# Kernel tuning notes

Measured on AMD Instinct MI355X. Metric: run time of the kernel, lower is better.

Reference implementation:

```python
import jax, jax.numpy as jnp
import numpy as np


def setup_inputs() -> dict:
    key = jax.random.key(0)
    doc_embeddings = jax.random.normal(key, (16384, 128), dtype=jnp.float32)
    return {"doc_embeddings": doc_embeddings}


def reference(doc_embeddings) -> jnp.ndarray:
    n = doc_embeddings.shape[0]
    # [N, N] pairwise dot products
    scores = jnp.matmul(doc_embeddings, doc_embeddings.T)
    positive_scores = jnp.diagonal(scores)  # [N]
    # zero out the diagonal (matches dot - eye*dot in the torch code)
    diag_mask = jnp.eye(n, dtype=scores.dtype)
    negative_scores = scores - diag_mask * scores
    positive_loss = jax.nn.log_sigmoid(positive_scores)            # [N]
    negative_loss = jax.nn.log_sigmoid(-negative_scores).sum(axis=1)  # [N]
    loss = -(positive_loss + negative_loss).mean()
    return loss
```

## Files before the change

### kernel.cpp

```cpp
#include <hip/hip_runtime.h>
#include <hip/hip_bf16.h>


#define N_DOCS 16384
#define DIM 128
#define NTILE 128
#define NTRI (NTILE * (NTILE + 1) / 2)
#define PBLOCKS 768

typedef __attribute__((ext_vector_type(4))) float f32x4;
typedef __attribute__((ext_vector_type(8))) __bf16 bf16x8;
typedef __attribute__((ext_vector_type(2))) long longx2;

typedef const __attribute__((address_space(1))) unsigned char* gptr_t;
typedef __attribute__((address_space(3))) unsigned char* lptr_t;

#define SQRT_LOG2E 1.2011224087864498f
#define LN2F 0.6931471805599453f
#define QC0 1.33985f
#define QC1 (-0.33985f)

#if __has_builtin(__builtin_amdgcn_exp2f)
#define EXP2F(x) __builtin_amdgcn_exp2f(x)
#else
#define EXP2F(x) exp2f(x)
#endif

#if __has_builtin(__builtin_amdgcn_mfma_scale_f32_16x16x128_f8f6f4)
#define HAVE_MX 1
typedef __attribute__((ext_vector_type(8))) int i32x8;
#endif

#define BARRIER() do { asm volatile("" ::: "memory"); \
                       __builtin_amdgcn_s_barrier();  \
                       asm volatile("" ::: "memory"); } while (0)

__device__ __forceinline__ unsigned short f2bf(float f) {
  unsigned int u = __float_as_uint(f);
  u += 0x7fffu + ((u >> 16) & 1u);
  return (unsigned short)(u >> 16);
}

#if __has_builtin(__builtin_amdgcn_cvt_pk_fp8_f32)
#define HAVE_CVT_FP8 1
#else
__device__ __forceinline__ unsigned char f2e4m3(float x) {
  unsigned int u = __float_as_uint(x);
  unsigned char sgn = (unsigned char)((u >> 31) << 7);
  float ax = fabsf(x);
  if (!(ax < 464.f)) return sgn | 0x7E;
  unsigned int ua = u & 0x7FFFFFFFu;
  int e = (int)(ua >> 23) - 127;
  if (e < -6) {
    float q = rintf(ax * 512.f);
    return sgn | (unsigned char)q;
  }
  unsigned int mant = ua & 0x7FFFFFu;
  unsigned int keep = mant >> 20;
  unsigned int rest = mant & 0xFFFFFu;
  keep += (rest > 0x80000u) || (rest == 0x80000u && (keep & 1u));
  unsigned int ee = (unsigned int)(e + 7);
  if (keep == 8u) { keep = 0u; ee++; }
  if (ee >= 16u) return sgn | 0x7E;
  return sgn | (unsigned char)((ee << 3) | keep);
}
#endif

__device__ __forceinline__ void tri_decode(int g, int& tr, int& tc) {
  int r = (int)((2 * NTILE + 1 -
                 sqrtf((float)((2 * NTILE + 1) * (2 * NTILE + 1)) - 8.0f * (float)g)) * 0.5f);
  while (r * NTILE - r * (r - 1) / 2 > g) --r;
  while ((r + 1) * NTILE - (r + 1) * r / 2 <= g) ++r;
  tr = r;
  tc = r + (g - (r * NTILE - r * (r - 1) / 2));
}

__global__ __launch_bounds__(256) void cast_kernel(const float* __restrict__ in,
                                                   unsigned char* __restrict__ out,
                                                   float* __restrict__ rpart,
                                                   float* __restrict__ colpart,
                                                   float* __restrict__ accum,
                                                   unsigned int* __restrict__ counter) {
  __shared__ float cs[16][136];
  __shared__ float redr[4];
  const int b = blockIdx.x, tid = threadIdx.x;
  const int kb = tid & 15, rg = tid >> 4;
  if (b == 0 && tid == 0) { accum[0] = 0.f; *counter = 0u; }

  float csum[8] = {0.f, 0.f, 0.f, 0.f, 0.f, 0.f, 0.f, 0.f};
  float rsum = 0.f;
#pragma unroll
  for (int it = 0; it < 8; ++it) {
    int r = it * 16 + rg;
    int row = b * 128 + r;
    const float4* p = reinterpret_cast<const float4*>(in + (size_t)row * 128 + kb * 8);
    float4 a = p[0], c = p[1];
    float v0 = a.x * SQRT_LOG2E, v1 = a.y * SQRT_LOG2E, v2 = a.z * SQRT_LOG2E,
          v3 = a.w * SQRT_LOG2E, v4 = c.x * SQRT_LOG2E, v5 = c.y * SQRT_LOG2E,
          v6 = c.z * SQRT_LOG2E, v7 = c.w * SQRT_LOG2E;
    int w0, w1;
#ifdef HAVE_CVT_FP8
    w0 = __builtin_amdgcn_cvt_pk_fp8_f32(v0, v1, 0, false);
    w0 = __builtin_amdgcn_cvt_pk_fp8_f32(v2, v3, w0, true);
    w1 = __builtin_amdgcn_cvt_pk_fp8_f32(v4, v5, 0, false);
    w1 = __builtin_amdgcn_cvt_pk_fp8_f32(v6, v7, w1, true);
#else
    w0 = (int)f2e4m3(v0) | ((int)f2e4m3(v1) << 8) | ((int)f2e4m3(v2) << 16) | ((int)f2e4m3(v3) << 24);
    w1 = (int)f2e4m3(v4) | ((int)f2e4m3(v5) << 8) | ((int)f2e4m3(v6) << 16) | ((int)f2e4m3(v7) << 24);
#endif
    int g = kb & 3, s = kb >> 2;
    int off = b * 16384 + (g * 2 + (s >> 1)) * 2048 + r * 16 + (s & 1) * 8;
    *reinterpret_cast<int2*>(out + off) = make_int2(w0, w1);
    csum[0] += v0; csum[1] += v1; csum[2] += v2; csum[3] += v3;
    csum[4] += v4; csum[5] += v5; csum[6] += v6; csum[7] += v7;
    rsum = fmaf(v0, v0, rsum); rsum = fmaf(v1, v1, rsum);
    rsum = fmaf(v2, v2, rsum); rsum = fmaf(v3, v3, rsum);
    rsum = fmaf(v4, v4, rsum); rsum = fmaf(v5, v5, rsum);
    rsum = fmaf(v6, v6, rsum); rsum = fmaf(v7, v7, rsum);
  }
#pragma unroll
  for (int j = 0; j < 8; ++j) cs[rg][kb * 8 + j] = csum[j];
#pragma unroll
  for (int off = 32; off > 0; off >>= 1) rsum += __shfl_down(rsum, off);
  if ((tid & 63) == 0) redr[tid >> 6] = rsum;
  __syncthreads();
  if (tid < 128) {
    float s = 0.f;
#pragma unroll
    for (int r = 0; r < 16; ++r) s += cs[r][tid];
    colpart[b * 128 + tid] = s;
  }
  if (tid == 0) rpart[b] = redr[0] + redr[1] + redr[2] + redr[3];
}

__global__ __launch_bounds__(512, 6) void loss_persist(const unsigned char* __restrict__ ef8,
                                                       float* __restrict__ accum,
                                                       unsigned int* __restrict__ counter,
                                                       const float* __restrict__ rpart,
                                                       const float* __restrict__ colpart,
                                                       float* __restrict__ out) {
  __shared__ alignas(16) unsigned char Asl[16384];
  __shared__ alignas(16) unsigned char Bsl[2][16384];
  __shared__ float red[8];
  __shared__ int lastFlag;
  const int tid = threadIdx.x;
  const int p = blockIdx.x;
  const int g0 = (p * 43) >> 2;
  const int g1 = ((p + 1) * 43) >> 2;
  const int n = g1 - g0;

  const int wid = tid >> 6;
  const int lane = tid & 63;
  const int wm = wid >> 2, wn = wid & 3;
  const int lrow = lane & 15;
  const int kgrp = lane >> 4;

  auto stageA = [&](int t) {
    const unsigned char* s = ef8 + (size_t)t * 16384;
#pragma unroll
    for (int it = 0; it < 2; ++it) {
      int pp = (it * 512 + tid) * 16;
      __builtin_amdgcn_global_load_lds((gptr_t)(s + pp), (lptr_t)(Asl + pp), 16, 0, 0);
    }
  };
  auto stageB = [&](int t, int buf) {
    const unsigned char* s = ef8 + (size_t)t * 16384;
#pragma unroll
    for (int it = 0; it < 2; ++it) {
      int pp = (it * 512 + tid) * 16;
      __builtin_amdgcn_global_load_lds((gptr_t)(s + pp), (lptr_t)(Bsl[buf] + pp), 16, 0, 0);
    }
  };

  auto compute = [&](int buf) -> float {
    const unsigned char* As = (const unsigned char*)Asl;
    const unsigned char* Bs = (const unsigned char*)Bsl[buf];

    f32x4 acc[4][2];
#pragma unroll
    for (int a = 0; a < 4; ++a)
#pragma unroll
      for (int c = 0; c < 2; ++c) acc[a][c] = (f32x4){0.f, 0.f, 0.f, 0.f};

#ifdef HAVE_MX
    const int pbase = kgrp * 2 * 2048;
    i32x8 b8[2];
#pragma unroll
    for (int f = 0; f < 2; ++f) {
      int br = wn * 32 + f * 16 + lrow;
      int4 lo = *reinterpret_cast<const int4*>(Bs + pbase + br * 16);
      int4 hi = *reinterpret_cast<const int4*>(Bs + pbase + 2048 + br * 16);
      b8[f] = (i32x8){lo.x, lo.y, lo.z, lo.w, hi.x, hi.y, hi.z, hi.w};
    }
    __builtin_amdgcn_s_setprio(1);
#pragma unroll
    for (int fm = 0; fm < 4; ++fm) {
      int ar = wm * 64 + fm * 16 + lrow;
      int4 lo = *reinterpret_cast<const int4*>(As + pbase + ar * 16);
      int4 hi = *reinterpret_cast<const int4*>(As + pbase + 2048 + ar * 16);
      i32x8 a8 = (i32x8){lo.x, lo.y, lo.z, lo.w, hi.x, hi.y, hi.z, hi.w};
#pragma unroll
      for (int fn = 0; fn < 2; ++fn)
        acc[fm][fn] = __builtin_amdgcn_mfma_scale_f32_16x16x128_f8f6f4(
            a8, b8[fn], acc[fm][fn], 0, 0, 0, 127, 0, 127);
    }
    __builtin_amdgcn_s_setprio(0);
#else
#pragma unroll
    for (int ks2 = 0; ks2 < 2; ++ks2) {
      longx2 af[4], bf[2];
      const int pbase = (kgrp * 2 + ks2) * 2048;
#pragma unroll
      for (int f = 0; f < 4; ++f) {
        int ar = wm * 64 + f * 16 + lrow;
        af[f] = *reinterpret_cast<const longx2*>(As + pbase + ar * 16);
      }
#pragma unroll
      for (int f = 0; f < 2; ++f) {
        int br = wn * 32 + f * 16 + lrow;
        bf[f] = *reinterpret_cast<const longx2*>(Bs + pbase + br * 16);
      }
      __builtin_amdgcn_s_setprio(1);
#pragma unroll
      for (int fm = 0; fm < 4; ++fm)
#pragma unroll
        for (int fn = 0; fn < 2; ++fn) {
          acc[fm][fn] = __builtin_amdgcn_mfma_f32_16x16x32_fp8_fp8(af[fm].x, bf[fn].x,
                                                                   acc[fm][fn], 0, 0, 0);
          acc[fm][fn] = __builtin_amdgcn_mfma_f32_16x16x32_fp8_fp8(af[fm].y, bf[fn].y,
                                                                   acc[fm][fn], 0, 0, 0);
        }
      __builtin_amdgcn_s_setprio(0);
    }
#endif

    float sa = 0.f, su = 0.f;
#pragma unroll
    for (int fm = 0; fm < 4; ++fm)
#pragma unroll
      for (int fn = 0; fn < 2; ++fn)
#pragma unroll
        for (int r = 0; r < 4; ++r) {
          float a = fabsf(acc[fm][fn][r]);
          sa += a;
          float u = EXP2F(-a);
          su = fmaf(u, fmaf(u, QC1, QC0), su);
        }
    return fmaf(0.5f, sa, su);
  };

  int tr, tc;
  tri_decode(g0, tr, tc);
  float total = 0.f;
  int buf = 0;
  stageA(tr);
  stageB(tc, 0);
  for (int i = 0; i < n; ++i) {
    int ntr = tr, ntc = tc + 1;
    if (ntc == NTILE) { ntr = tr + 1; ntc = ntr; }
    const bool have_next = (i + 1 < n);
    const bool samerow = have_next && (ntr == tr);
    if (samerow) {
      stageB(ntc, buf ^ 1);
      asm volatile("s_waitcnt vmcnt(2)" ::: "memory");
    } else {
      asm volatile("s_waitcnt vmcnt(0)" ::: "memory");
    }
    BARRIER();
    total += (tr == tc ? 1.f : 2.f) * compute(buf);
    BARRIER();
    if (have_next && !samerow) {
      stageA(ntr);
      stageB(ntc, buf ^ 1);
    }
    tr = ntr; tc = ntc; buf ^= 1;
  }

#pragma unroll
  for (int off = 32; off > 0; off >>= 1) total += __shfl_down(total, off);
  if (lane == 0) red[wid] = total;
  __syncthreads();
  if (tid == 0) {
    float t = red[0] + red[1] + red[2] + red[3] + red[4] + red[5] + red[6] + red[7];
    atomicAdd(accum, t);
    __threadfence();
    unsigned int old = atomicAdd(counter, 1u);
    lastFlag = (old == (unsigned int)(PBLOCKS - 1));
  }
  __syncthreads();
  if (lastFlag) {
    float part = 0.f;
    if (tid < 128) {
      float cs = 0.f;
#pragma unroll 8
      for (int b = 0; b < 128; ++b) cs += colpart[b * 128 + tid];
      part = fmaf(0.5f * cs, cs, -rpart[tid]);
#pragma unroll
      for (int off = 32; off > 0; off >>= 1) part += __shfl_down(part, off);
      if (lane == 0) red[wid] = part;
    }
    __syncthreads();
    if (tid == 0) {
      float tail = red[0] + red[1];
      float acc = atomicAdd(accum, 0.f);
      out[0] = LN2F * ((acc + tail) * (1.0f / (float)N_DOCS) + 1.0f);
    }
  }
}

__global__ __launch_bounds__(512, 2) void loss_fallback(const float* __restrict__ src,
                                                        float* __restrict__ accum) {
  const int b = blockIdx.x;
  int tr, tc;
  tri_decode(b, tr, tc);

  __shared__ alignas(16) unsigned short As[128 * 128];
  __shared__ alignas(16) unsigned short Bs[128 * 128];
  __shared__ float red[8];
  const int tid = threadIdx.x;

  const float4* srcA4 = (const float4*)(src + (size_t)tr * 16384);
  const float4* srcB4 = (const float4*)(src + (size_t)tc * 16384);
#pragma unroll
  for (int it = 0; it < 8; ++it) {
    int idx = it * 512 + tid;
    int L = idx * 8;
    int swz = L ^ (((L >> 8) & 7) << 4);
    float4 a = srcA4[idx];
    ushort4 oa = {f2bf(a.x * SQRT_LOG2E), f2bf(a.y * SQRT_LOG2E),
                  f2bf(a.z * SQRT_LOG2E), f2bf(a.w * SQRT_LOG2E)};
    *reinterpret_cast<ushort4*>((unsigned char*)As + swz) = oa;
    float4 bb = srcB4[idx];
    ushort4 ob = {f2bf(bb.x * SQRT_LOG2E), f2bf(bb.y * SQRT_LOG2E),
                  f2bf(bb.z * SQRT_LOG2E), f2bf(bb.w * SQRT_LOG2E)};
    *reinterpret_cast<ushort4*>((unsigned char*)Bs + swz) = ob;
  }
  __syncthreads();

  const int wid = tid >> 6;
  const int lane = tid & 63;
  const int wm = wid >> 2, wn = wid & 3;
  const int lrow = lane & 15;
  const int kgrp = lane >> 4;

  f32x4 acc[4][2];
#pragma unroll
  for (int a = 0; a < 4; ++a)
#pragma unroll
    for (int c = 0; c < 2; ++c) acc[a][c] = (f32x4){0.f, 0.f, 0.f, 0.f};

#pragma unroll
  for (int ks = 0; ks < 4; ++ks) {
    bf16x8 af[4], bfr[2];
#pragma unroll
    for (int f = 0; f < 4; ++f) {
      int ar = wm * 64 + f * 16 + lrow;
      int ab = (ar * 256 + ks * 64 + kgrp * 16) ^ ((ar & 7) << 4);
      af[f] = *reinterpret_cast<const bf16x8*>((const unsigned char*)As + ab);
    }
#pragma unroll
    for (int f = 0; f < 2; ++f) {
      int br = wn * 32 + f * 16 + lrow;
      int bb = (br * 256 + ks * 64 + kgrp * 16) ^ ((br & 7) << 4);
      bfr[f] = *reinterpret_cast<const bf16x8*>((const unsigned char*)Bs + bb);
    }
#pragma unroll
    for (int fm = 0; fm < 4; ++fm)
#pragma unroll
      for (int fn = 0; fn < 2; ++fn)
        acc[fm][fn] = __builtin_amdgcn_mfma_f32_16x16x32_bf16(af[fm], bfr[fn], acc[fm][fn], 0, 0, 0);
  }

  float sm = 0.f, sp = 0.f;
  if (tr == tc) {
#pragma unroll
    for (int fm = 0; fm < 4; ++fm)
#pragma unroll
      for (int fn = 0; fn < 2; ++fn)
#pragma unroll
        for (int r = 0; r < 4; ++r) {
          float v = acc[fm][fn][r];
          int il = wm * 64 + fm * 16 + kgrp * 4 + r;
          int jl = wn * 32 + fn * 16 + lrow;
          if (il == jl) v = -v;
          sm += fmaxf(v, 0.f);
          float u = EXP2F(-fabsf(v));
          sp = fmaf(u, fmaf(u, QC1, QC0), sp);
        }
  } else {
#pragma unroll
    for (int fm = 0; fm < 4; ++fm)
#pragma unroll
      for (int fn = 0; fn < 2; ++fn)
#pragma unroll
        for (int r = 0; r < 4; ++r) {
          float v = acc[fm][fn][r];
          sm += fmaxf(v, 0.f);
          float u = EXP2F(-fabsf(v));
          sp = fmaf(u, fmaf(u, QC1, QC0), sp);
        }
    sm *= 2.f;
    sp *= 2.f;
  }

  float lsum = sm + sp;
#pragma unroll
  for (int off = 32; off > 0; off >>= 1) lsum += __shfl_down(lsum, off);
  if (lane == 0) red[wid] = lsum;
  __syncthreads();
  if (tid == 0) {
    float t = red[0] + red[1] + red[2] + red[3] + red[4] + red[5] + red[6] + red[7];
    atomicAdd(accum, t);
  }
}

__global__ void finalize_kernel(const float* __restrict__ accum, float* __restrict__ out) {
  out[0] = LN2F * (accum[0] * (1.0f / (float)N_DOCS) + 1.0f);
}

extern "C" void kernel_launch(void* const* d_in, const int* in_sizes, int n_in,
                              void* d_out, int out_size, void* d_ws, size_t ws_size,
                              hipStream_t stream) {
  const float* E = (const float*)d_in[0];
  float* out = (float*)d_out;
  float* accum = (float*)d_ws;
  unsigned int* counter = (unsigned int*)((char*)d_ws + 64);
  float* rpart = (float*)((char*)d_ws + 256);
  float* colpart = (float*)((char*)d_ws + 1024);
  unsigned char* ef8 = (unsigned char*)d_ws + 66560;

  const size_t need = 66560 + (size_t)N_DOCS * DIM + 256;
  if (ws_size >= need) {
    cast_kernel<<<128, 256, 0, stream>>>(E, ef8, rpart, colpart, accum, counter);
    loss_persist<<<PBLOCKS, 512, 0, stream>>>(ef8, accum, counter, rpart, colpart, out);
  } else {
    (void)hipMemsetAsync(accum, 0, sizeof(float), stream);
    loss_fallback<<<NTRI, 512, 0, stream>>>(E, accum);
    finalize_kernel<<<1, 1, 0, stream>>>(accum, out);
  }
}
```

Before: 100.8 us.

## Read A tile directly from global, drop A LDS buffer, raise occupancy to 8 blocks

Removes the shared-memory A tile so each block's A fragments are loaded straight from global memory (through cache) inside compute. This shrinks LDS per block so the launch bound can go to 8 blocks/CU, and the persistent grid grows from 768 to 1024 blocks with a general triangle split. B stays double-buffered and is now prefetched across row changes too. The s_setprio hints around the MFMA loop in the non-MX path are removed. The trade-off is that A global loads now sit on the compute critical path and hit cache on every tile, which could stall MFMAs.

```diff
diff --git a/kernel.cpp b/kernel.cpp
--- a/kernel.cpp
+++ b/kernel.cpp
@@ -6,7 +6,7 @@
 #define DIM 128
 #define NTILE 128
 #define NTRI (NTILE * (NTILE + 1) / 2)
-#define PBLOCKS 768
+#define PBLOCKS 1024
 
 typedef __attribute__((ext_vector_type(4))) float f32x4;
 typedef __attribute__((ext_vector_type(8))) __bf16 bf16x8;
@@ -133,20 +133,19 @@
   if (tid == 0) rpart[b] = redr[0] + redr[1] + redr[2] + redr[3];
 }
 
-__global__ __launch_bounds__(512, 6) void loss_persist(const unsigned char* __restrict__ ef8,
+__global__ __launch_bounds__(512, 8) void loss_persist(const unsigned char* __restrict__ ef8,
                                                        float* __restrict__ accum,
                                                        unsigned int* __restrict__ counter,
                                                        const float* __restrict__ rpart,
                                                        const float* __restrict__ colpart,
                                                        float* __restrict__ out) {
-  __shared__ alignas(16) unsigned char Asl[16384];
   __shared__ alignas(16) unsigned char Bsl[2][16384];
   __shared__ float red[8];
   __shared__ int lastFlag;
   const int tid = threadIdx.x;
   const int p = blockIdx.x;
-  const int g0 = (p * 43) >> 2;
-  const int g1 = ((p + 1) * 43) >> 2;
+  const int g0 = (p * NTRI) / PBLOCKS;
+  const int g1 = ((p + 1) * NTRI) / PBLOCKS;
   const int n = g1 - g0;
 
   const int wid = tid >> 6;
@@ -155,14 +154,6 @@
   const int lrow = lane & 15;
   const int kgrp = lane >> 4;
 
-  auto stageA = [&](int t) {
-    const unsigned char* s = ef8 + (size_t)t * 16384;
-#pragma unroll
-    for (int it = 0; it < 2; ++it) {
-      int pp = (it * 512 + tid) * 16;
-      __builtin_amdgcn_global_load_lds((gptr_t)(s + pp), (lptr_t)(Asl + pp), 16, 0, 0);
-    }
-  };
   auto stageB = [&](int t, int buf) {
     const unsigned char* s = ef8 + (size_t)t * 16384;
 #pragma unroll
@@ -172,9 +163,9 @@
     }
   };
 
-  auto compute = [&](int buf) -> float {
-    const unsigned char* As = (const unsigned char*)Asl;
+  auto compute = [&](int buf, int tr) -> float {
     const unsigned char* Bs = (const unsigned char*)Bsl[buf];
+    const unsigned char* Ag = ef8 + (size_t)tr * 16384;
 
     f32x4 acc[4][2];
 #pragma unroll
@@ -183,7 +174,7 @@
       for (int c = 0; c < 2; ++c) acc[a][c] = (f32x4){0.f, 0.f, 0.f, 0.f};
 
 #ifdef HAVE_MX
-    const int pbase = kgrp * 2 * 2048;
+    const int pbase = kgrp * 4096;
     i32x8 b8[2];
 #pragma unroll
     for (int f = 0; f < 2; ++f) {
@@ -196,8 +187,8 @@
 #pragma unroll
     for (int fm = 0; fm < 4; ++fm) {
       int ar = wm * 64 + fm * 16 + lrow;
-      int4 lo = *reinterpret_cast<const int4*>(As + pbase + ar * 16);
-      int4 hi = *reinterpret_cast<const int4*>(As + pbase + 2048 + ar * 16);
+      int4 lo = *reinterpret_cast<const int4*>(Ag + pbase + ar * 16);
+      int4 hi = *reinterpret_cast<const int4*>(Ag + pbase + 2048 + ar * 16);
       i32x8 a8 = (i32x8){lo.x, lo.y, lo.z, lo.w, hi.x, hi.y, hi.z, hi.w};
 #pragma unroll
       for (int fn = 0; fn < 2; ++fn)
@@ -213,14 +204,13 @@
 #pragma unroll
       for (int f = 0; f < 4; ++f) {
         int ar = wm * 64 + f * 16 + lrow;
-        af[f] = *reinterpret_cast<const longx2*>(As + pbase + ar * 16);
+        af[f] = *reinterpret_cast<const longx2*>(Ag + pbase + ar * 16);
       }
 #pragma unroll
       for (int f = 0; f < 2; ++f) {
         int br = wn * 32 + f * 16 + lrow;
         bf[f] = *reinterpret_cast<const longx2*>(Bs + pbase + br * 16);
       }
-      __builtin_amdgcn_s_setprio(1);
 #pragma unroll
       for (int fm = 0; fm < 4; ++fm)
 #pragma unroll
@@ -230,7 +220,6 @@
           acc[fm][fn] = __builtin_amdgcn_mfma_f32_16x16x32_fp8_fp8(af[fm].y, bf[fn].y,
                                                                    acc[fm][fn], 0, 0, 0);
         }
-      __builtin_amdgcn_s_setprio(0);
     }
 #endif
 
@@ -253,26 +242,19 @@
   tri_decode(g0, tr, tc);
   float total = 0.f;
   int buf = 0;
-  stageA(tr);
   stageB(tc, 0);
   for (int i = 0; i < n; ++i) {
     int ntr = tr, ntc = tc + 1;
     if (ntc == NTILE) { ntr = tr + 1; ntc = ntr; }
-    const bool have_next = (i + 1 < n);
-    const bool samerow = have_next && (ntr == tr);
-    if (samerow) {
+    if (i + 1 < n) {
       stageB(ntc, buf ^ 1);
       asm volatile("s_waitcnt vmcnt(2)" ::: "memory");
     } else {
       asm volatile("s_waitcnt vmcnt(0)" ::: "memory");
     }
     BARRIER();
-    total += (tr == tc ? 1.f : 2.f) * compute(buf);
+    total += (tr == tc ? 1.f : 2.f) * compute(buf, tr);
     BARRIER();
-    if (have_next && !samerow) {
-      stageA(ntr);
-      stageB(ntc, buf ^ 1);
-    }
     tr = ntr; tc = ntc; buf ^= 1;
   }
 
```

After: 108.6 us. +7.7%, slower.
